# Kernel tuning notes

Measured on AMD Instinct MI355X. Metric: run time of the kernel, lower is better.

The kernel has to match this reference:

```python
import jax, jax.numpy as jnp
import numpy as np

PATCH = 32        # max_patch_size == patch_stride == gate dim
LEVELS = 3        # n_real_experts; patch sizes 32 -> 16 -> 8
N_REAL = 3
N_NULL = 1
N_EXPERTS = N_REAL + N_NULL
K = 2             # n_activated_experts
ROUTE_SCALE = 1.0
SEQ_LEN = 2097152


def setup_inputs():
    key = jax.random.key(0)
    kx, kw = jax.random.split(key)
    x = jax.random.normal(kx, (1, SEQ_LEN), dtype=jnp.float32)
    mask = jnp.ones((1, SEQ_LEN), dtype=jnp.float32)
    Wg = jax.random.normal(kw, (N_EXPERTS, PATCH), dtype=jnp.float32) * 0.02
    return {"x": x, "mask": mask, "Wg": Wg}


def _route_structure(scores_np):
    """Concrete (non-differentiable) routing / split structure.
    scores_np: [P, E] gate softmax scores. Returns top-k ids, parent map,
    gather positions, validity mask, final sizes, granularity mask."""
    idx = np.argsort(-scores_np, axis=-1)[:, :K]                 # top-k expert ids [P,K]
    masked = np.where(idx < N_REAL, idx, -1)
    lvl = masked.max(axis=-1)
    lvl = np.maximum(lvl, 0)                                     # null-expert-only -> level 0
    counts = (1 << lvl).astype(np.int64)                         # each patch -> 2**lvl children
    P = scores_np.shape[0]
    total = int(counts.sum())
    parent = np.repeat(np.arange(P), counts)                     # [T] original patch id
    starts = np.cumsum(counts) - counts
    c = np.arange(total) - np.repeat(starts, counts)             # chunk index within parent
    v = lvl[parent]                                              # split level of each final patch
    sz = (PATCH >> v).astype(np.int64)                           # final patch length
    t = np.arange(PATCH)[None, :]
    valid = (t < sz[:, None])
    pos = np.where(valid, c[:, None] * sz[:, None] + t, 0)       # gather offsets in parent block
    # granularity mask: ones at own chunk at own level, and containing chunk one level coarser
    g = np.zeros((total, LEVELS, PATCH), np.float32)
    own = ((t >= (c * sz)[:, None]) & (t < ((c + 1) * sz)[:, None])).astype(np.float32)
    g[np.arange(total), v] = own
    hp = v >= 1
    szp = PATCH >> np.maximum(v - 1, 0)
    cp = c // 2
    par = ((t >= (cp * szp)[:, None]) & (t < ((cp + 1) * szp)[:, None])).astype(np.float32)
    g[np.arange(total)[hp], (v - 1)[hp]] = par[hp]
    return idx, parent, pos, valid, sz, g


def reference(x, mask, Wg):
    # non-overlapping patchify (stride == patch size)
    xp = x.reshape(-1, PATCH)                                    # [P, PATCH]
    mp = mask.reshape(-1, PATCH)
    scores = jax.nn.softmax(xp @ Wg.T, axis=-1)                  # [P, E] gate scores
    idx_np, parent, pos, valid, sz, g = _route_structure(np.asarray(scores))
    idx = jnp.asarray(idx_np)
    w_top = jnp.take_along_axis(scores, idx, axis=-1) * ROUTE_SCALE   # [P, K]
    parent_j = jnp.asarray(parent)
    pos_j = jnp.asarray(pos)
    valid_f = jnp.asarray(valid.astype(np.float32))
    xg = xp[parent_j]                                            # parent blocks [T, PATCH]
    mg = mp[parent_j]                                            # parent block masks
    new_x = jnp.take_along_axis(xg, pos_j, axis=1) * valid_f     # left-aligned, zero padded
    new_mask = jnp.take_along_axis(mg, pos_j, axis=1) * valid_f
    new_size = jnp.asarray(sz.astype(np.int32))                  # [T]
    weights = w_top[parent_j]                                    # children inherit routing [T,K]
    expert_idx = idx[parent_j]                                   # [T,K]
    gran = jnp.asarray(g)                                        # [T, LEVELS, PATCH]
    x_final = xg[:, None, :] * gran * mg[:, None, :]             # [T, LEVELS, PATCH]
    return (new_x[None], new_mask[None], new_size[None],
            weights[None], expert_idx[None], x_final[None])
```

## Files before the change

### kernel.cpp

```cpp
#include <hip/hip_runtime.h>

#define PATCH 32
#define FLAGRDY (1 << 30)
#define SUMMASK 0xFFFFFF

typedef float f4 __attribute__((ext_vector_type(4)));

__device__ __forceinline__ f4 to_f4(const float4 v) {
    f4 r; r.x = v.x; r.y = v.y; r.z = v.z; r.w = v.w; return r;
}

__global__ __launch_bounds__(256) void k_fused(
    const float* __restrict__ x, const float* __restrict__ mask,
    const float* __restrict__ Wg,
    int* __restrict__ flags,
    float* __restrict__ o_newx, float* __restrict__ o_newm,
    float* __restrict__ o_size, float* __restrict__ o_w,
    float* __restrict__ o_eidx, float* __restrict__ o_xf)
{
    __shared__ float sw[128];
    __shared__ int   sc[256];
    __shared__ int   sMeta[256];
    __shared__ float sW0[256], sW1[256];
    __shared__ int   sRowP[1024];
    __shared__ int   sOffS;

    const int tid = threadIdx.x;
    const int bid = blockIdx.x;
    if (tid < 128) sw[tid] = Wg[tid];

    const long pbase = (long)bid * (256 * PATCH);
    const float4* x4 = (const float4*)(x + pbase);
    const float4* m4 = (const float4*)(mask + pbase);
    float4 xv[8];
    #pragma unroll
    for (int i = 0; i < 8; i++) xv[i] = x4[tid * 8 + i];
    __syncthreads();

    float z0 = 0.f, z1 = 0.f, z2 = 0.f, z3 = 0.f;
    #pragma unroll
    for (int i = 0; i < 8; i++) {
        const float4 f = xv[i];
        const int i4 = i * 4;
        z0 = fmaf(f.x, sw[i4],      z0); z0 = fmaf(f.y, sw[i4+1],      z0);
        z0 = fmaf(f.z, sw[i4+2],    z0); z0 = fmaf(f.w, sw[i4+3],      z0);
        z1 = fmaf(f.x, sw[32+i4],   z1); z1 = fmaf(f.y, sw[32+i4+1],   z1);
        z1 = fmaf(f.z, sw[32+i4+2], z1); z1 = fmaf(f.w, sw[32+i4+3],   z1);
        z2 = fmaf(f.x, sw[64+i4],   z2); z2 = fmaf(f.y, sw[64+i4+1],   z2);
        z2 = fmaf(f.z, sw[64+i4+2], z2); z2 = fmaf(f.w, sw[64+i4+3],   z2);
        z3 = fmaf(f.x, sw[96+i4],   z3); z3 = fmaf(f.y, sw[96+i4+1],   z3);
        z3 = fmaf(f.z, sw[96+i4+2], z3); z3 = fmaf(f.w, sw[96+i4+3],   z3);
    }
    const float zm = fmaxf(fmaxf(z0, z1), fmaxf(z2, z3));
    const float e0 = expf(z0 - zm), e1 = expf(z1 - zm),
                e2 = expf(z2 - zm), e3 = expf(z3 - zm);
    const float s = e0 + e1 + e2 + e3;
    float pv[4];
    pv[0] = e0 / s; pv[1] = e1 / s; pv[2] = e2 / s; pv[3] = e3 / s;

    int b0 = 0; float v0 = pv[0];
    #pragma unroll
    for (int i = 1; i < 4; i++) if (pv[i] > v0) { v0 = pv[i]; b0 = i; }
    int b1 = -1; float v1 = -1.f;
    #pragma unroll
    for (int i = 0; i < 4; i++) if (i != b0 && pv[i] > v1) { v1 = pv[i]; b1 = i; }

    const int m0 = (b0 < 3) ? b0 : -1;
    const int m1 = (b1 < 3) ? b1 : -1;
    int lv = m0 > m1 ? m0 : m1;
    if (lv < 0) lv = 0;
    const int cnt = 1 << lv;

    sMeta[tid] = b0 | (b1 << 4) | (lv << 8);
    sW0[tid] = v0;
    sW1[tid] = v1;

    sc[tid] = cnt;
    __syncthreads();
    for (int off = 1; off < 256; off <<= 1) {
        const int t = (tid >= off) ? sc[tid - off] : 0;
        __syncthreads();
        sc[tid] += t;
        __syncthreads();
    }
    const int lst = sc[tid] - cnt;

    if (tid == 255)
        __hip_atomic_store(&flags[bid], FLAGRDY | sc[255],
                           __ATOMIC_RELAXED, __HIP_MEMORY_SCOPE_AGENT);

    for (int c = 0; c < cnt; c++) sRowP[lst + c] = (tid << 2) | c;

    if (tid < 64) {
        int acc = 0;
        for (int b = tid; b < bid; b += 64) {
            int f;
            while ((((f = __hip_atomic_load(&flags[b], __ATOMIC_RELAXED,
                                            __HIP_MEMORY_SCOPE_AGENT))) & FLAGRDY) == 0)
                __builtin_amdgcn_s_sleep(4);
            acc += f & SUMMASK;
        }
        #pragma unroll
        for (int off = 32; off >= 1; off >>= 1) acc += __shfl_down(acc, off);
        if (tid == 0) sOffS = acc;
    }
    __syncthreads();

    const int  bs = sc[255];
    const long R0 = sOffS;

    for (int g = tid; g < bs; g += 256) {
        const int jp = sRowP[g] >> 2;
        const int v = (sMeta[jp] >> 8) & 15;
        __builtin_nontemporal_store((float)(PATCH >> v), &o_size[R0 + g]);
    }
    for (int g = tid; g < 2 * bs; g += 256) {
        const int row = g >> 1, k = g & 1;
        const int jp = sRowP[row] >> 2;
        const int mt = sMeta[jp];
        const float wv = k ? sW1[jp] : sW0[jp];
        const float ev = (float)(k ? ((mt >> 4) & 15) : (mt & 15));
        __builtin_nontemporal_store(wv, &o_w[R0 * 2 + g]);
        __builtin_nontemporal_store(ev, &o_eidx[R0 * 2 + g]);
    }

    f4* __restrict__ onx = (f4*)o_newx + R0 * 8;
    f4* __restrict__ onm = (f4*)o_newm + R0 * 8;
    for (int g = tid; g < bs * 8; g += 256) {
        const int row = g >> 3, q = g & 7;
        const int rp = sRowP[row];
        const int jp = rp >> 2, c = rp & 3;
        const int sz = PATCH >> ((sMeta[jp] >> 8) & 15);
        f4 vx = {0.f, 0.f, 0.f, 0.f}, vm = {0.f, 0.f, 0.f, 0.f};
        if (4 * q < sz) {
            const int off = jp * 8 + ((c * sz) >> 2) + q;
            vx = to_f4(x4[off]);
            vm = to_f4(m4[off]);
        }
        __builtin_nontemporal_store(vx, &onx[g]);
        __builtin_nontemporal_store(vm, &onm[g]);
    }

    f4* __restrict__ oxf = (f4*)o_xf + R0 * 24;
    for (int g = tid; g < bs * 24; g += 256) {
        const int row = g / 24;
        const int rem = g - row * 24;
        const int l = rem >> 3, q = rem & 7;
        const int rp = sRowP[row];
        const int jp = rp >> 2, c = rp & 3;
        const int v = (sMeta[jp] >> 8) & 15;
        const int sz = PATCH >> v;
        const int t4 = 4 * q;
        bool nz = false;
        if (l == v) {
            const int lo = c * sz;
            nz = (t4 >= lo) && (t4 < lo + sz);
        } else if (v >= 1 && l == v - 1) {
            const int cp = c >> 1, szp = sz << 1, lo = cp * szp;
            nz = (t4 >= lo) && (t4 < lo + szp);
        }
        f4 o = {0.f, 0.f, 0.f, 0.f};
        if (nz) {
            const int off = jp * 8 + q;
            const float4 a = x4[off], b = m4[off];
            o.x = a.x * b.x; o.y = a.y * b.y;
            o.z = a.z * b.z; o.w = a.w * b.w;
        }
        __builtin_nontemporal_store(o, &oxf[g]);
    }
}

extern "C" void kernel_launch(void* const* d_in, const int* in_sizes, int n_in,
                              void* d_out, int out_size, void* d_ws, size_t ws_size,
                              hipStream_t stream) {
    const float* x    = (const float*)d_in[0];
    const float* mask = (const float*)d_in[1];
    const float* Wg   = (const float*)d_in[2];

    const int  P  = in_sizes[0] / PATCH;
    const int  NB = (P + 255) / 256;
    const long T  = (long)out_size / 165;

    int* flags = (int*)d_ws;

    float* out = (float*)d_out;
    float* o_newx = out;
    float* o_newm = out + T * 32;
    float* o_size = out + T * 64;
    float* o_w    = out + T * 65;
    float* o_eidx = out + T * 67;
    float* o_xf   = out + T * 69;

    (void)hipMemsetAsync(flags, 0, (size_t)NB * sizeof(int), stream);
    hipLaunchKernelGGL(k_fused, dim3(NB), dim3(256), 0, stream,
                       x, mask, Wg, flags,
                       o_newx, o_newm, o_size, o_w, o_eidx, o_xf);
}
```

Baseline: 175.1 us.

## Shrink blocks to 32 patches with 8 threads per patch gate dot

Each block now handles 32 patches instead of 256, so 8 threads cooperate on one patch's gate dot product and combine partials with xor shuffles. The intra-block scan becomes a single-wavefront shuffle scan. The cross-block decoupled lookback now has 256 threads polling flags and accumulating through a shared atomic. Launch bounds request 4 blocks per CU. This raises parallelism and occupancy for the gate and scan phases, but gives 8x more blocks and a much longer serial lookback chain. It also drops handling of a partial last block.

New measurement: 160.5 us. 1.09x faster.

```diff
diff --git a/kernel.cpp b/kernel.cpp
--- a/kernel.cpp
+++ b/kernel.cpp
@@ -1,6 +1,7 @@
 #include <hip/hip_runtime.h>
 
 #define PATCH 32
+#define PPB   32
 #define FLAGRDY (1 << 30)
 #define SUMMASK 0xFFFFFF
 
@@ -10,7 +11,7 @@
     f4 r; r.x = v.x; r.y = v.y; r.z = v.z; r.w = v.w; return r;
 }
 
-__global__ __launch_bounds__(256) void k_fused(
+__global__ __launch_bounds__(256, 4) void k_fused(
     const float* __restrict__ x, const float* __restrict__ mask,
     const float* __restrict__ Wg,
     int* __restrict__ flags,
@@ -19,106 +20,110 @@
     float* __restrict__ o_eidx, float* __restrict__ o_xf)
 {
     __shared__ float sw[128];
-    __shared__ int   sc[256];
-    __shared__ int   sMeta[256];
-    __shared__ float sW0[256], sW1[256];
-    __shared__ int   sRowP[1024];
+    __shared__ int   sMeta[PPB];
+    __shared__ float sW0[PPB], sW1[PPB];
+    __shared__ int   sCnt[PPB];
+    __shared__ int   sLst[PPB];
+    __shared__ int   sRowP[PPB * 4];
     __shared__ int   sOffS;
+    __shared__ int   sTot;
 
     const int tid = threadIdx.x;
     const int bid = blockIdx.x;
     if (tid < 128) sw[tid] = Wg[tid];
-
-    const long pbase = (long)bid * (256 * PATCH);
+    if (tid == 0) sOffS = 0;
+
+    const long pbase = (long)bid * (PPB * PATCH);
     const float4* x4 = (const float4*)(x + pbase);
     const float4* m4 = (const float4*)(mask + pbase);
-    float4 xv[8];
+
+    const int jp = tid >> 3, sub = tid & 7;
+    const float4 xq = x4[tid];
+    __syncthreads();
+
+    const int k4 = sub * 4;
+    float z0 = fmaf(xq.x, sw[k4],    fmaf(xq.y, sw[k4+1],    fmaf(xq.z, sw[k4+2],    xq.w * sw[k4+3])));
+    float z1 = fmaf(xq.x, sw[32+k4], fmaf(xq.y, sw[32+k4+1], fmaf(xq.z, sw[32+k4+2], xq.w * sw[32+k4+3])));
+    float z2 = fmaf(xq.x, sw[64+k4], fmaf(xq.y, sw[64+k4+1], fmaf(xq.z, sw[64+k4+2], xq.w * sw[64+k4+3])));
+    float z3 = fmaf(xq.x, sw[96+k4], fmaf(xq.y, sw[96+k4+1], fmaf(xq.z, sw[96+k4+2], xq.w * sw[96+k4+3])));
     #pragma unroll
-    for (int i = 0; i < 8; i++) xv[i] = x4[tid * 8 + i];
+    for (int mm = 1; mm < 8; mm <<= 1) {
+        z0 += __shfl_xor(z0, mm);
+        z1 += __shfl_xor(z1, mm);
+        z2 += __shfl_xor(z2, mm);
+        z3 += __shfl_xor(z3, mm);
+    }
+    if (sub == 0) {
+        const float zm = fmaxf(fmaxf(z0, z1), fmaxf(z2, z3));
+        const float e0 = expf(z0 - zm), e1 = expf(z1 - zm),
+                    e2 = expf(z2 - zm), e3 = expf(z3 - zm);
+        const float s = e0 + e1 + e2 + e3;
+        float pv[4];
+        pv[0] = e0 / s; pv[1] = e1 / s; pv[2] = e2 / s; pv[3] = e3 / s;
+
+        int b0 = 0; float v0 = pv[0];
+        #pragma unroll
+        for (int i = 1; i < 4; i++) if (pv[i] > v0) { v0 = pv[i]; b0 = i; }
+        int b1 = -1; float v1 = -1.f;
+        #pragma unroll
+        for (int i = 0; i < 4; i++) if (i != b0 && pv[i] > v1) { v1 = pv[i]; b1 = i; }
+
+        const int m0 = (b0 < 3) ? b0 : -1;
+        const int m1 = (b1 < 3) ? b1 : -1;
+        int lv = m0 > m1 ? m0 : m1;
+        if (lv < 0) lv = 0;
+
+        sMeta[jp] = b0 | (b1 << 4) | (lv << 8);
+        sW0[jp] = v0;
+        sW1[jp] = v1;
+        sCnt[jp] = 1 << lv;
+    }
     __syncthreads();
 
-    float z0 = 0.f, z1 = 0.f, z2 = 0.f, z3 = 0.f;
+    if (tid < PPB) {
+        const int c = sCnt[tid];
+        int inc = c;
+        #pragma unroll
+        for (int d = 1; d < PPB; d <<= 1) {
+            const int t = __shfl_up(inc, d);
+            if (tid >= d) inc += t;
+        }
+        const int lst = inc - c;
+        sLst[tid] = lst;
+        if (tid == PPB - 1) {
+            sTot = inc;
+            __hip_atomic_store(&flags[bid], FLAGRDY | inc,
+                               __ATOMIC_RELAXED, __HIP_MEMORY_SCOPE_AGENT);
+        }
+        for (int c2 = 0; c2 < c; c2++) sRowP[lst + c2] = (tid << 2) | c2;
+    }
+
+    int acc = 0;
+    for (int b = tid; b < bid; b += 256) {
+        int f;
+        while (((f = __hip_atomic_load(&flags[b], __ATOMIC_RELAXED,
+                                       __HIP_MEMORY_SCOPE_AGENT)) & FLAGRDY) == 0)
+            __builtin_amdgcn_s_sleep(2);
+        acc += f & SUMMASK;
+    }
     #pragma unroll
-    for (int i = 0; i < 8; i++) {
-        const float4 f = xv[i];
-        const int i4 = i * 4;
-        z0 = fmaf(f.x, sw[i4],      z0); z0 = fmaf(f.y, sw[i4+1],      z0);
-        z0 = fmaf(f.z, sw[i4+2],    z0); z0 = fmaf(f.w, sw[i4+3],      z0);
-        z1 = fmaf(f.x, sw[32+i4],   z1); z1 = fmaf(f.y, sw[32+i4+1],   z1);
-        z1 = fmaf(f.z, sw[32+i4+2], z1); z1 = fmaf(f.w, sw[32+i4+3],   z1);
-        z2 = fmaf(f.x, sw[64+i4],   z2); z2 = fmaf(f.y, sw[64+i4+1],   z2);
-        z2 = fmaf(f.z, sw[64+i4+2], z2); z2 = fmaf(f.w, sw[64+i4+3],   z2);
-        z3 = fmaf(f.x, sw[96+i4],   z3); z3 = fmaf(f.y, sw[96+i4+1],   z3);
-        z3 = fmaf(f.z, sw[96+i4+2], z3); z3 = fmaf(f.w, sw[96+i4+3],   z3);
-    }
-    const float zm = fmaxf(fmaxf(z0, z1), fmaxf(z2, z3));
-    const float e0 = expf(z0 - zm), e1 = expf(z1 - zm),
-                e2 = expf(z2 - zm), e3 = expf(z3 - zm);
-    const float s = e0 + e1 + e2 + e3;
-    float pv[4];
-    pv[0] = e0 / s; pv[1] = e1 / s; pv[2] = e2 / s; pv[3] = e3 / s;
-
-    int b0 = 0; float v0 = pv[0];
-    #pragma unroll
-    for (int i = 1; i < 4; i++) if (pv[i] > v0) { v0 = pv[i]; b0 = i; }
-    int b1 = -1; float v1 = -1.f;
-    #pragma unroll
-    for (int i = 0; i < 4; i++) if (i != b0 && pv[i] > v1) { v1 = pv[i]; b1 = i; }
-
-    const int m0 = (b0 < 3) ? b0 : -1;
-    const int m1 = (b1 < 3) ? b1 : -1;
-    int lv = m0 > m1 ? m0 : m1;
-    if (lv < 0) lv = 0;
-    const int cnt = 1 << lv;
-
-    sMeta[tid] = b0 | (b1 << 4) | (lv << 8);
-    sW0[tid] = v0;
-    sW1[tid] = v1;
-
-    sc[tid] = cnt;
+    for (int off = 32; off >= 1; off >>= 1) acc += __shfl_down(acc, off);
+    if ((tid & 63) == 0 && acc) atomicAdd(&sOffS, acc);
     __syncthreads();
-    for (int off = 1; off < 256; off <<= 1) {
-        const int t = (tid >= off) ? sc[tid - off] : 0;
-        __syncthreads();
-        sc[tid] += t;
-        __syncthreads();
-    }
-    const int lst = sc[tid] - cnt;
-
-    if (tid == 255)
-        __hip_atomic_store(&flags[bid], FLAGRDY | sc[255],
-                           __ATOMIC_RELAXED, __HIP_MEMORY_SCOPE_AGENT);
-
-    for (int c = 0; c < cnt; c++) sRowP[lst + c] = (tid << 2) | c;
-
-    if (tid < 64) {
-        int acc = 0;
-        for (int b = tid; b < bid; b += 64) {
-            int f;
-            while ((((f = __hip_atomic_load(&flags[b], __ATOMIC_RELAXED,
-                                            __HIP_MEMORY_SCOPE_AGENT))) & FLAGRDY) == 0)
-                __builtin_amdgcn_s_sleep(4);
-            acc += f & SUMMASK;
-        }
-        #pragma unroll
-        for (int off = 32; off >= 1; off >>= 1) acc += __shfl_down(acc, off);
-        if (tid == 0) sOffS = acc;
-    }
-    __syncthreads();
-
-    const int  bs = sc[255];
+
+    const int  bs = sTot;
     const long R0 = sOffS;
 
     for (int g = tid; g < bs; g += 256) {
-        const int jp = sRowP[g] >> 2;
-        const int v = (sMeta[jp] >> 8) & 15;
+        const int jq = sRowP[g] >> 2;
+        const int v = (sMeta[jq] >> 8) & 15;
         __builtin_nontemporal_store((float)(PATCH >> v), &o_size[R0 + g]);
     }
     for (int g = tid; g < 2 * bs; g += 256) {
         const int row = g >> 1, k = g & 1;
-        const int jp = sRowP[row] >> 2;
-        const int mt = sMeta[jp];
-        const float wv = k ? sW1[jp] : sW0[jp];
+        const int jq = sRowP[row] >> 2;
+        const int mt = sMeta[jq];
+        const float wv = k ? sW1[jq] : sW0[jq];
         const float ev = (float)(k ? ((mt >> 4) & 15) : (mt & 15));
         __builtin_nontemporal_store(wv, &o_w[R0 * 2 + g]);
         __builtin_nontemporal_store(ev, &o_eidx[R0 * 2 + g]);
@@ -129,11 +134,11 @@
     for (int g = tid; g < bs * 8; g += 256) {
         const int row = g >> 3, q = g & 7;
         const int rp = sRowP[row];
-        const int jp = rp >> 2, c = rp & 3;
-        const int sz = PATCH >> ((sMeta[jp] >> 8) & 15);
+        const int jq = rp >> 2, c = rp & 3;
+        const int sz = PATCH >> ((sMeta[jq] >> 8) & 15);
         f4 vx = {0.f, 0.f, 0.f, 0.f}, vm = {0.f, 0.f, 0.f, 0.f};
         if (4 * q < sz) {
-            const int off = jp * 8 + ((c * sz) >> 2) + q;
+            const int off = jq * 8 + ((c * sz) >> 2) + q;
             vx = to_f4(x4[off]);
             vm = to_f4(m4[off]);
         }
@@ -147,8 +152,8 @@
         const int rem = g - row * 24;
         const int l = rem >> 3, q = rem & 7;
         const int rp = sRowP[row];
-        const int jp = rp >> 2, c = rp & 3;
-        const int v = (sMeta[jp] >> 8) & 15;
+        const int jq = rp >> 2, c = rp & 3;
+        const int v = (sMeta[jq] >> 8) & 15;
         const int sz = PATCH >> v;
         const int t4 = 4 * q;
         bool nz = false;
@@ -161,7 +166,7 @@
         }
         f4 o = {0.f, 0.f, 0.f, 0.f};
         if (nz) {
-            const int off = jp * 8 + q;
+            const int off = jq * 8 + q;
             const float4 a = x4[off], b = m4[off];
             o.x = a.x * b.x; o.y = a.y * b.y;
             o.z = a.z * b.z; o.w = a.w * b.w;
@@ -177,9 +182,9 @@
     const float* mask = (const float*)d_in[1];
     const float* Wg   = (const float*)d_in[2];
 
-    const int  P  = in_sizes[0] / PATCH;
-    const int  NB = (P + 255) / 256;
-    const long T  = (long)out_size / 165;
+    const int  P   = in_sizes[0] / PATCH;
+    const int  NB  = P / PPB;
+    const long T   = (long)out_size / 165;
 
     int* flags = (int*)d_ws;
 
```
